# Kernel tuning notes

Hardware: AMD Instinct MI355X
Metric: run time of the kernel (lower is better)

The kernel has to match this reference:

```python
import math
import jax, jax.numpy as jnp
import numpy as np

C = 256          # channels
HID = 64         # max(int(C*0.25),16)
RH = 64          # max(C//4,32) router hidden
N, S, H, W = 8, 64, 16, 16
LOW_FREQ_RATIO = 0.2
ROUTER_TEMP = 1.0
LN_EPS = 1e-5

def gelu(v):
    return jax.nn.gelu(v, approximate=False)

def bn1d(v, s, b):  # folded eval-mode BatchNorm1d: (N,C,S)
    return v * s[None, :, None] + b[None, :, None]

def conv1x1(v, w, b=None):  # v:(N,Cin,S), w:(Cout,Cin)
    o = jnp.einsum('oc,ncs->nos', w, v)
    if b is not None:
        o = o + b[None, :, None]
    return o

def convk(v, w):  # v:(N,Cin,S), w:(Cout,Cin,K), 'same' padding
    k = w.shape[-1]
    return jax.lax.conv_general_dilated(v, w, (1,), [(k // 2, k // 2)],
                                        dimension_numbers=('NCH', 'OIH', 'NCH'))

def setup_inputs():
    key = jax.random.key(0)
    ks = iter(jax.random.split(key, 64))
    def nrm(shape, sc=0.02):
        return jax.random.normal(next(ks), shape, jnp.float32) * sc
    d = {}
    d['x'] = jax.random.normal(next(ks), (N, C, S, H, W), jnp.float32)
    d['ln_g'] = jnp.ones((C,), jnp.float32)
    d['ln_b'] = jnp.zeros((C,), jnp.float32)
    for k in (3, 5, 7):
        d['mb_w%d' % k] = nrm((C, 3 * C, k))
        d['mb_s%d' % k] = 1.0 + nrm((C,))
        d['mb_b%d' % k] = nrm((C,))
    d['mf_w'] = nrm((C, C)); d['mf_s'] = 1.0 + nrm((C,)); d['mf_b'] = nrm((C,))
    d['pg_w1'] = nrm((HID, 3)); d['pg_s1'] = 1.0 + nrm((HID,)); d['pg_b1'] = nrm((HID,))
    d['pg_w2'] = nrm((C, HID)); d['pg_b2'] = nrm((C,))
    d['pp_w'] = nrm((C, C)); d['pp_s'] = 1.0 + nrm((C,)); d['pp_b'] = nrm((C,))
    d['mg_w'] = nrm((C, 2 * C)); d['mg_b'] = nrm((C,))
    d['mo_w1'] = nrm((C, 3 * C)); d['mo_s1'] = 1.0 + nrm((C,)); d['mo_b1'] = nrm((C,))
    d['mo_w2'] = nrm((C, C))
    d['rt_w1'] = nrm((RH, C + 5)); d['rt_b1'] = nrm((RH,))
    d['rt_w2'] = nrm((3, RH)); d['rt_b2'] = nrm((3,))
    d['bp_w1'] = nrm((C, 4 * C)); d['bp_s1'] = 1.0 + nrm((C,)); d['bp_b1'] = nrm((C,))
    d['bp_w2'] = nrm((C, C))
    d['res_scale'] = jnp.full((1, C, 1), 0.05, jnp.float32)
    d['fg_w'] = nrm((C, C)); d['fg_b'] = nrm((C,))
    d['sg_w'] = nrm((C, C)); d['sg_s'] = 1.0 + nrm((C,)); d['sg_b'] = nrm((C,))
    return d

def _forward(x, ln_g, ln_b, mb_w3, mb_s3, mb_b3, mb_w5, mb_s5, mb_b5,
             mb_w7, mb_s7, mb_b7, mf_w, mf_s, mf_b,
             pg_w1, pg_s1, pg_b1, pg_w2, pg_b2, pp_w, pp_s, pp_b,
             mg_w, mg_b, mo_w1, mo_s1, mo_b1, mo_w2,
             rt_w1, rt_b1, rt_w2, rt_b2, bp_w1, bp_s1, bp_b1, bp_w2,
             res_scale, fg_w, fg_b, sg_w, sg_s, sg_b):
    n, c, s = x.shape[:3]
    x32 = x.astype(jnp.float32)
    desc = x32.mean(axis=(-1, -2))                     # (N,C,S)
    t = desc.transpose(0, 2, 1)                        # (N,S,C)
    mu = t.mean(-1, keepdims=True)
    var = t.var(-1, keepdims=True)
    dn = (((t - mu) / jnp.sqrt(var + LN_EPS)) * ln_g + ln_b).transpose(0, 2, 1)  # (N,C,S)

    def tdiff(v, order):
        dd = v[:, :, order:] - v[:, :, :-order]
        return jnp.pad(dd, ((0, 0), (0, 0), (order, 0)))
    diff1 = tdiff(dn, 1)
    diff2 = tdiff(dn, 2)

    # motion branch (multi-kernel conv1d + BN + GELU)
    mi = jnp.concatenate([dn, diff1, diff2], axis=1)   # (N,3C,S)
    motion = 0.0
    for w, bs, bb in ((mb_w3, mb_s3, mb_b3), (mb_w5, mb_s5, mb_b5), (mb_w7, mb_s7, mb_b7)):
        motion = motion + gelu(bn1d(convk(mi, w), bs, bb))
    motion = gelu(bn1d(conv1x1(motion / 3.0, mf_w), mf_s, mf_b))

    # FFT-based cycle / phase estimation
    tokens = dn.transpose(0, 2, 1)                     # (N,S,C)
    freq = jnp.fft.rfft(tokens, axis=1, norm='ortho')  # (N,F,C) complex
    fe = jnp.abs(freq).mean(-1)                        # (N,F)
    Fb = fe.shape[1]
    low = min(max(int(round(Fb * LOW_FREQ_RATIO)), 1), Fb - 1)
    he = fe[:, low:]
    peak_rel = jnp.argmax(he, axis=-1)                 # (N,)
    peak_idx = peak_rel + low
    peak_val = jnp.take_along_axis(he, peak_rel[:, None], axis=1)
    cycle_conf = peak_val / jnp.maximum(he.sum(axis=1, keepdims=True), 1e-6)  # (N,1)
    peak_norm = peak_idx.astype(jnp.float32)[:, None] / float(Fb - 1)
    mean_freq = freq.mean(-1)                          # (N,F) complex
    dom = jnp.take_along_axis(mean_freq, peak_idx[:, None], axis=1)[:, 0]
    dom_phase = jnp.arctan2(dom.imag, dom.real)
    tax = jnp.arange(s, dtype=jnp.float32)
    ang = (2.0 * math.pi / max(s, 1)) * peak_idx.astype(jnp.float32)
    arg = ang[:, None] * tax[None, :] + dom_phase[:, None]
    phase_cos = jnp.cos(arg)[:, None, :]               # (N,1,S)
    phase_sin = jnp.sin(arg)[:, None, :]

    cycle_token = jnp.broadcast_to(cycle_conf[:, :, None], (n, 1, s))
    pf = jnp.concatenate([phase_cos, phase_sin, cycle_token], axis=1)  # (N,3,S)
    pgate = jax.nn.sigmoid(conv1x1(gelu(bn1d(conv1x1(pf, pg_w1), pg_s1, pg_b1)), pg_w2, pg_b2))
    phase = gelu(bn1d(conv1x1(dn * pgate, pp_w), pp_s, pp_b))

    # bidirectional EMA memory via lax.scan
    gate = jax.nn.sigmoid(conv1x1(jnp.concatenate([dn, jnp.abs(diff1)], axis=1), mg_w, mg_b))
    g = gate.transpose(2, 0, 1)                        # (S,N,C)
    dd = dn.transpose(2, 0, 1)
    def step(st, gd):
        gt, dt = gd
        st = gt * st + (1.0 - gt) * dt
        return st, st
    _, fo = jax.lax.scan(step, dd[0], (g[1:], dd[1:]))
    fwd_mem = jnp.concatenate([dd[:1], fo], axis=0).transpose(1, 2, 0)
    _, bo = jax.lax.scan(step, dd[-1], (g[-2::-1], dd[-2::-1]))
    bwd_mem = jnp.concatenate([dd[-1:], bo], axis=0)[::-1].transpose(1, 2, 0)
    memory = conv1x1(gelu(bn1d(conv1x1(
        jnp.concatenate([dn, fwd_mem, bwd_mem], axis=1), mo_w1), mo_s1, mo_b1)), mo_w2)

    # router
    seq_std = dn.std(axis=2).mean(axis=1, keepdims=True)
    diff_energy = jnp.abs(diff1).mean(axis=(1, 2))[:, None]
    motion_energy = jnp.abs(motion).mean(axis=(1, 2))[:, None]
    memory_energy = jnp.abs(memory - dn).mean(axis=(1, 2))[:, None]
    stats = jnp.concatenate([seq_std, diff_energy, cycle_conf, peak_norm,
                             memory_energy + motion_energy], axis=-1)
    ri = jnp.concatenate([dn.mean(-1), stats], axis=-1)  # (N,C+5)
    hdn = gelu(ri @ rt_w1.T + rt_b1)
    logits = hdn @ rt_w2.T + rt_b2
    bw = jax.nn.softmax(logits / max(ROUTER_TEMP, 1e-6), axis=-1)  # (N,3)
    fused = (bw[:, 0, None, None] * motion + bw[:, 1, None, None] * phase
             + bw[:, 2, None, None] * memory)

    delta = conv1x1(gelu(bn1d(conv1x1(
        jnp.concatenate([dn, fused, motion - phase, memory - dn], axis=1),
        bp_w1), bp_s1, bp_b1)), bp_w2)
    delta = delta * jax.nn.sigmoid(conv1x1(dn, fg_w, fg_b))
    delta = res_scale * delta
    delta = delta[:, :, :, None, None]                 # (N,C,S,1,1)

    sp = x32.mean(axis=2)                              # (N,C,H,W)
    sg_lin = jnp.einsum('oc,nchw->nohw', sg_w, sp)
    sgate = jax.nn.sigmoid(sg_lin * sg_s[None, :, None, None] + sg_b[None, :, None, None])
    delta = delta * sgate[:, :, None, :, :]            # (N,C,S,H,W)
    return x + delta.astype(x.dtype)

def reference(x, ln_g, ln_b, mb_w3, mb_s3, mb_b3, mb_w5, mb_s5, mb_b5,
              mb_w7, mb_s7, mb_b7, mf_w, mf_s, mf_b,
              pg_w1, pg_s1, pg_b1, pg_w2, pg_b2, pp_w, pp_s, pp_b,
              mg_w, mg_b, mo_w1, mo_s1, mo_b1, mo_w2,
              rt_w1, rt_b1, rt_w2, rt_b2, bp_w1, bp_s1, bp_b1, bp_w2,
              res_scale, fg_w, fg_b, sg_w, sg_s, sg_b):
    return _forward(x, ln_g, ln_b, mb_w3, mb_s3, mb_b3, mb_w5, mb_s5, mb_b5,
                    mb_w7, mb_s7, mb_b7, mf_w, mf_s, mf_b,
                    pg_w1, pg_s1, pg_b1, pg_w2, pg_b2, pp_w, pp_s, pp_b,
                    mg_w, mg_b, mo_w1, mo_s1, mo_b1, mo_w2,
                    rt_w1, rt_b1, rt_w2, rt_b2, bp_w1, bp_s1, bp_b1, bp_w2,
                    res_scale, fg_w, fg_b, sg_w, sg_s, sg_b)
```

## Files before the change

### kernel.cpp

```cpp
#include <hip/hip_runtime.h>
#include <math.h>

namespace {

constexpr int N_ = 8, C_ = 256, S_ = 64, HW_ = 256;
constexpr int NS = N_ * S_;
constexpr int NHW = N_ * HW_;

constexpr size_t SZ_DESC = (size_t)NS * C_;
constexpr size_t O_DESC = 0;
constexpr size_t O_DN   = O_DESC + SZ_DESC;
constexpr size_t SZ_MIC = (size_t)N_ * 768 * 80;
constexpr size_t O_MIC  = O_DN + SZ_DESC;
constexpr size_t SZ_MPRE = (size_t)3 * 4 * 2048 * 64;
constexpr size_t O_MPRE = O_MIC + SZ_MIC;
constexpr size_t O_MSUM = O_MPRE + SZ_MPRE;
constexpr size_t O_MOT  = O_MSUM + SZ_DESC;
constexpr size_t SZ_GIB = (size_t)NS * 512;
constexpr size_t O_GIB  = O_MOT + SZ_DESC;
constexpr size_t O_GATE = O_GIB + SZ_GIB;
constexpr size_t SZ_MOI = (size_t)NS * 768;
constexpr size_t O_MOI  = O_GATE + SZ_DESC;
constexpr size_t O_HMO  = O_MOI + SZ_MOI;
constexpr size_t O_MEM  = O_HMO + SZ_DESC;
constexpr size_t O_PPIN = O_MEM + SZ_DESC;
constexpr size_t O_PHASE= O_PPIN + SZ_DESC;
constexpr size_t O_FGATE= O_PHASE + SZ_DESC;
constexpr size_t SZ_BPI = (size_t)NS * 1024;
constexpr size_t O_BPI  = O_FGATE + SZ_DESC;
constexpr size_t O_HBP  = O_BPI + SZ_BPI;
constexpr size_t O_DELTA= O_HBP + SZ_DESC;
constexpr size_t SZ_SPT = (size_t)NHW * C_;
constexpr size_t O_SPT  = O_DELTA + SZ_DESC;
constexpr size_t O_SGATE= O_SPT + SZ_SPT;
constexpr size_t O_FE   = O_SGATE + SZ_SPT;
constexpr size_t O_MFRE = O_FE + 512;
constexpr size_t O_MFIM = O_MFRE + 512;
constexpr size_t O_PK   = O_MFIM + 512;
constexpr size_t O_BW   = O_PK + 32;
constexpr size_t SZ_WT3 = (size_t)768*3*256;
constexpr size_t O_WT3  = O_BW + 32;
constexpr size_t SZ_WT5 = (size_t)768*5*256;
constexpr size_t O_WT5  = O_WT3 + SZ_WT3;
constexpr size_t SZ_WT7 = (size_t)768*7*256;
constexpr size_t O_WT7  = O_WT5 + SZ_WT5;
constexpr size_t O_ATMF = O_WT7 + SZ_WT7;
constexpr size_t O_ATMG = O_ATMF + 256*256;
constexpr size_t O_ATMO1= O_ATMG + 512*256;
constexpr size_t O_ATMO2= O_ATMO1 + 768*256;
constexpr size_t O_ATPP = O_ATMO2 + 256*256;
constexpr size_t O_ATBP1= O_ATPP + 256*256;
constexpr size_t O_ATBP2= O_ATBP1 + 1024*256;
constexpr size_t O_ATFG = O_ATBP2 + 256*256;
constexpr size_t O_ATSG = O_ATFG + 256*256;

__device__ __forceinline__ float gelu_f(float v) {
  return 0.5f * v * (1.0f + erff(v * 0.70710678118654752f));
}
__device__ __forceinline__ float sigmoid_f(float v) {
  return 1.0f / (1.0f + expf(-v));
}

__device__ __forceinline__ float block_sum256(float v, float* scratch) {
  #pragma unroll
  for (int off = 32; off; off >>= 1) v += __shfl_down(v, off, 64);
  int w = threadIdx.x >> 6;
  __syncthreads();
  if ((threadIdx.x & 63) == 0) scratch[w] = v;
  __syncthreads();
  return scratch[0] + scratch[1] + scratch[2] + scratch[3];
}

__global__ __launch_bounds__(256) void transpose_kernel(
    const float* __restrict__ w3, const float* __restrict__ w5, const float* __restrict__ w7,
    const float* __restrict__ wmf, const float* __restrict__ wmg,
    const float* __restrict__ wmo1, const float* __restrict__ wmo2,
    const float* __restrict__ wpp, const float* __restrict__ wbp1,
    const float* __restrict__ wbp2, const float* __restrict__ wfg,
    const float* __restrict__ wsg, float* __restrict__ ws) {
  __shared__ float tile[32][33];
  int xt = blockIdx.x, yt = blockIdx.y;
  const float* src; float* dst; int K;
  if      (xt < 72)  { src = w3;   dst = ws + O_WT3;   K = 2304; }
  else if (xt < 192) { src = w5;   dst = ws + O_WT5;   K = 3840; xt -= 72; }
  else if (xt < 360) { src = w7;   dst = ws + O_WT7;   K = 5376; xt -= 192; }
  else if (xt < 368) { src = wmf;  dst = ws + O_ATMF;  K = 256;  xt -= 360; }
  else if (xt < 384) { src = wmg;  dst = ws + O_ATMG;  K = 512;  xt -= 368; }
  else if (xt < 408) { src = wmo1; dst = ws + O_ATMO1; K = 768;  xt -= 384; }
  else if (xt < 416) { src = wmo2; dst = ws + O_ATMO2; K = 256;  xt -= 408; }
  else if (xt < 424) { src = wpp;  dst = ws + O_ATPP;  K = 256;  xt -= 416; }
  else if (xt < 456) { src = wbp1; dst = ws + O_ATBP1; K = 1024; xt -= 424; }
  else if (xt < 464) { src = wbp2; dst = ws + O_ATBP2; K = 256;  xt -= 456; }
  else if (xt < 472) { src = wfg;  dst = ws + O_ATFG;  K = 256;  xt -= 464; }
  else               { src = wsg;  dst = ws + O_ATSG;  K = 256;  xt -= 472; }
  int tx = threadIdx.x & 31, ty = threadIdx.x >> 5;
  int c = xt * 32 + tx;
  #pragma unroll
  for (int i = 0; i < 4; ++i) {
    int r = yt * 32 + ty + i * 8;
    tile[ty + i * 8][tx] = src[(size_t)r * K + c];
  }
  __syncthreads();
  #pragma unroll
  for (int i = 0; i < 4; ++i) {
    int cc = xt * 32 + ty + i * 8;
    dst[(size_t)cc * 256 + yt * 32 + tx] = tile[tx][ty + i * 8];
  }
}

__global__ __launch_bounds__(256) void reduce_x_kernel(
    const float* __restrict__ x, float* __restrict__ desc_t, float* __restrict__ sp_t) {
  int nc = blockIdx.x; int n = nc >> 8; int c = nc & 255;
  int t = threadIdx.x; int w = t >> 6; int l = t & 63;
  const float4* x4 = (const float4*)x + (size_t)nc * 4096;
  float4 sa = {0.f, 0.f, 0.f, 0.f};
  for (int i = 0; i < 16; ++i) {
    int s = w * 16 + i;
    float4 v = x4[(size_t)s * 64 + l];
    sa.x += v.x; sa.y += v.y; sa.z += v.z; sa.w += v.w;
    float ds = v.x + v.y + v.z + v.w;
    #pragma unroll
    for (int off = 32; off; off >>= 1) ds += __shfl_down(ds, off, 64);
    if (l == 0) desc_t[((size_t)n * 64 + s) * 256 + c] = ds * (1.f / 256.f);
  }
  __shared__ float4 lsp[4][64];
  lsp[w][l] = sa;
  __syncthreads();
  if (t < 64) {
    float4 a = lsp[0][t], b = lsp[1][t], c2 = lsp[2][t], d = lsp[3][t];
    float4 tot;
    tot.x = a.x + b.x + c2.x + d.x; tot.y = a.y + b.y + c2.y + d.y;
    tot.z = a.z + b.z + c2.z + d.z; tot.w = a.w + b.w + c2.w + d.w;
    size_t base = ((size_t)n * 256 + t * 4) * 256 + c;
    sp_t[base]       = tot.x * (1.f / 64.f);
    sp_t[base + 256] = tot.y * (1.f / 64.f);
    sp_t[base + 512] = tot.z * (1.f / 64.f);
    sp_t[base + 768] = tot.w * (1.f / 64.f);
  }
}

__global__ __launch_bounds__(256) void ln_kernel(
    const float* __restrict__ desc_t, const float* __restrict__ g,
    const float* __restrict__ b, float* __restrict__ dn_t) {
  __shared__ float sc[4];
  int col = blockIdx.x; int t = threadIdx.x;
  float v = desc_t[(size_t)col * 256 + t];
  float s1 = block_sum256(v, sc);
  float s2 = block_sum256(v * v, sc);
  float mu = s1 * (1.f / 256.f);
  float var = s2 * (1.f / 256.f) - mu * mu;
  float r = rsqrtf(var + 1e-5f);
  dn_t[(size_t)col * 256 + t] = (v - mu) * r * g[t] + b[t];
}

__global__ __launch_bounds__(256) void prep_mi_kernel(
    const float* __restrict__ dn_t, float* __restrict__ mi_c,
    float* __restrict__ gib, float* __restrict__ moi, float* __restrict__ bpi) {
  int col = blockIdx.x; int c = threadIdx.x;
  int n = col >> 6, s = col & 63;
  float d = dn_t[(size_t)col * 256 + c];
  float d1 = (s >= 1) ? d - dn_t[(size_t)(col - 1) * 256 + c] : 0.f;
  float d2 = (s >= 2) ? d - dn_t[(size_t)(col - 2) * 256 + c] : 0.f;
  size_t r0 = ((size_t)n * 768 + c) * 80;
  size_t r1 = ((size_t)n * 768 + 256 + c) * 80;
  size_t r2 = ((size_t)n * 768 + 512 + c) * 80;
  mi_c[r0 + 8 + s] = d; mi_c[r1 + 8 + s] = d1; mi_c[r2 + 8 + s] = d2;
  if (s < 8)  { mi_c[r0 + s] = 0.f; mi_c[r1 + s] = 0.f; mi_c[r2 + s] = 0.f; }
  if (s >= 56){ int p = 72 + (s - 56); mi_c[r0 + p] = 0.f; mi_c[r1 + p] = 0.f; mi_c[r2 + p] = 0.f; }
  gib[(size_t)col * 512 + c] = d;
  gib[(size_t)col * 512 + 256 + c] = fabsf(d1);
  moi[(size_t)col * 768 + c] = d;
  bpi[(size_t)col * 1024 + c] = d;
}

__global__ __launch_bounds__(256) void fft_kernel(
    const float* __restrict__ dn_t, float* __restrict__ fe,
    float* __restrict__ mfre, float* __restrict__ mfim) {
  int b = blockIdx.x; int n = b / 33; int f = b % 33;
  int t = threadIdx.x;
  __shared__ float cs[64], sn[64];
  __shared__ float sc[4];
  if (t < 64) {
    int ft = (f * t) & 63;
    float ang = -6.283185307179586f * (float)ft * (1.f / 64.f);
    cs[t] = cosf(ang); sn[t] = sinf(ang);
  }
  __syncthreads();
  float re = 0.f, im = 0.f;
  const float* base = dn_t + (size_t)n * 16384 + t;
  for (int s = 0; s < 64; ++s) {
    float v = base[(size_t)s * 256];
    re += v * cs[s]; im += v * sn[s];
  }
  re *= 0.125f; im *= 0.125f;
  float mag = sqrtf(re * re + im * im);
  float sm = block_sum256(mag, sc);
  float sr = block_sum256(re, sc);
  float si = block_sum256(im, sc);
  if (t == 0) {
    fe[b]   = sm * (1.f / 256.f);
    mfre[b] = sr * (1.f / 256.f);
    mfim[b] = si * (1.f / 256.f);
  }
}

__global__ __launch_bounds__(64) void peak_kernel(
    const float* __restrict__ fe, const float* __restrict__ mfre,
    const float* __restrict__ mfim, float* __restrict__ pk) {
  int n = blockIdx.x; int t = threadIdx.x;
  float v = (t < 26) ? fe[n * 33 + 7 + t] : -1e30f;
  int idx = t;
  float hs = (t < 26) ? v : 0.f;
  #pragma unroll
  for (int off = 32; off; off >>= 1) {
    float ov = __shfl_down(v, off, 64);
    int   oi = __shfl_down(idx, off, 64);
    float oh = __shfl_down(hs, off, 64);
    hs += oh;
    if (ov > v || (ov == v && oi < idx)) { v = ov; idx = oi; }
  }
  if (t == 0) {
    int pi = idx + 7;
    float conf = v / fmaxf(hs, 1e-6f);
    float pnorm = (float)pi * (1.f / 32.f);
    float re = mfre[n * 33 + pi], im = mfim[n * 33 + pi];
    float dph = atan2f(im, re);
    float ang = (6.283185307179586f / 64.f) * (float)pi;
    pk[n * 4 + 0] = conf; pk[n * 4 + 1] = pnorm; pk[n * 4 + 2] = dph; pk[n * 4 + 3] = ang;
  }
}

__global__ __launch_bounds__(256) void conv_fused_kernel(
    const float* __restrict__ mi_c, const float* __restrict__ wt3,
    const float* __restrict__ wt5, const float* __restrict__ wt7,
    float* __restrict__ mpre) {
  int n = blockIdx.x, part = blockIdx.y, ot = blockIdx.z;
  int t = threadIdx.x;
  __shared__ float lmi[192 * 80];
  {
    const float4* src = (const float4*)(mi_c + ((size_t)n * 768 + part * 192) * 80);
    float4* dst = (float4*)lmi;
    #pragma unroll
    for (int i = 0; i < 15; ++i) dst[t + i * 256] = src[t + i * 256];
  }
  __syncthreads();
  int o = ot * 32 + (t & 31);
  int s0 = (t >> 5) * 8;
  float a3[8], a5[8], a7[8];
  #pragma unroll
  for (int j = 0; j < 8; ++j) { a3[j] = 0.f; a5[j] = 0.f; a7[j] = 0.f; }
  const float* w3p = wt3 + (size_t)(part * 192 * 3) * 256 + o;
  const float* w5p = wt5 + (size_t)(part * 192 * 5) * 256 + o;
  const float* w7p = wt7 + (size_t)(part * 192 * 7) * 256 + o;
  const float* lrow = lmi + 8 + s0 - 3;
  for (int ic = 0; ic < 192; ++ic) {
    float win[14];
    #pragma unroll
    for (int j = 0; j < 14; ++j) win[j] = lrow[ic * 80 + j];
    #pragma unroll
    for (int dk = 0; dk < 7; ++dk) {
      float w = w7p[(size_t)(ic * 7 + dk) * 256];
      #pragma unroll
      for (int j = 0; j < 8; ++j) a7[j] = fmaf(w, win[dk + j], a7[j]);
    }
    #pragma unroll
    for (int dk = 0; dk < 5; ++dk) {
      float w = w5p[(size_t)(ic * 5 + dk) * 256];
      #pragma unroll
      for (int j = 0; j < 8; ++j) a5[j] = fmaf(w, win[1 + dk + j], a5[j]);
    }
    #pragma unroll
    for (int dk = 0; dk < 3; ++dk) {
      float w = w3p[(size_t)(ic * 3 + dk) * 256];
      #pragma unroll
      for (int j = 0; j < 8; ++j) a3[j] = fmaf(w, win[2 + dk + j], a3[j]);
    }
  }
  size_t base = ((size_t)part * 2048 + n * 256 + o) * 64 + s0;
  #pragma unroll
  for (int j = 0; j < 8; ++j) {
    mpre[base + j]           = a3[j];
    mpre[base + 524288 + j]  = a5[j];
    mpre[base + 1048576 + j] = a7[j];
  }
}

__global__ __launch_bounds__(256) void combine_kernel(
    const float* __restrict__ mpre,
    const float* __restrict__ s3, const float* __restrict__ b3,
    const float* __restrict__ s5, const float* __restrict__ b5,
    const float* __restrict__ s7, const float* __restrict__ b7,
    float* __restrict__ msum) {
  int id = blockIdx.x * 256 + threadIdx.x;
  int s = id & 63; int o = (id >> 6) & 255; int n = id >> 14;
  size_t base = ((size_t)n * 256 + o) * 64 + s;
  float v0 = mpre[base] + mpre[base + 131072] + mpre[base + 262144] + mpre[base + 393216];
  size_t b5o = base + 524288;
  float v1 = mpre[b5o] + mpre[b5o + 131072] + mpre[b5o + 262144] + mpre[b5o + 393216];
  size_t b7o = base + 1048576;
  float v2 = mpre[b7o] + mpre[b7o + 131072] + mpre[b7o + 262144] + mpre[b7o + 393216];
  float tot = gelu_f(v0 * s3[o] + b3[o]) + gelu_f(v1 * s5[o] + b5[o]) + gelu_f(v2 * s7[o] + b7[o]);
  msum[((size_t)n * 64 + s) * 256 + o] = tot * (1.f / 3.f);
}

template <int K, int EPI>
__global__ __launch_bounds__(256) void gemm_kernel(
    const float* __restrict__ At, const float* __restrict__ B, float* __restrict__ out,
    const float* __restrict__ sc, const float* __restrict__ bi,
    const float* __restrict__ fg, const float* __restrict__ rs) {
  int t = threadIdx.x;
  int o = blockIdx.x * 64 + (t & 63);
  int c0 = blockIdx.y * 8 + (t >> 6) * 2;
  const float* b0p = B + (size_t)c0 * K;
  const float* b1p = b0p + K;
  float4 a0 = {0.f,0.f,0.f,0.f}, a1 = {0.f,0.f,0.f,0.f};
  for (int kk = 0; kk < K; kk += 4) {
    float4 b0 = *(const float4*)(b0p + kk);
    float4 b1 = *(const float4*)(b1p + kk);
    float w0 = At[(size_t)(kk + 0) * 256 + o];
    float w1 = At[(size_t)(kk + 1) * 256 + o];
    float w2 = At[(size_t)(kk + 2) * 256 + o];
    float w3 = At[(size_t)(kk + 3) * 256 + o];
    a0.x += w0 * b0.x; a0.y += w1 * b0.y; a0.z += w2 * b0.z; a0.w += w3 * b0.w;
    a1.x += w0 * b1.x; a1.y += w1 * b1.y; a1.z += w2 * b1.z; a1.w += w3 * b1.w;
  }
  float v0 = (a0.x + a0.y) + (a0.z + a0.w);
  float v1 = (a1.x + a1.y) + (a1.z + a1.w);
  if constexpr (EPI == 0) { v0 = gelu_f(v0 * sc[o] + bi[o]); v1 = gelu_f(v1 * sc[o] + bi[o]); }
  else if constexpr (EPI == 1) { v0 = sigmoid_f(v0 + bi[o]); v1 = sigmoid_f(v1 + bi[o]); }
  else if constexpr (EPI == 3) {
    v0 *= fg[(size_t)c0 * 256 + o] * rs[o];
    v1 *= fg[(size_t)(c0 + 1) * 256 + o] * rs[o];
  }
  else if constexpr (EPI == 4) { v0 = sigmoid_f(v0 * sc[o] + bi[o]); v1 = sigmoid_f(v1 * sc[o] + bi[o]); }
  out[(size_t)c0 * 256 + o] = v0;
  out[(size_t)(c0 + 1) * 256 + o] = v1;
}

__global__ __launch_bounds__(256) void scan_kernel(
    const float* __restrict__ dn_t, const float* __restrict__ gate_t, float* __restrict__ moi) {
  int n = blockIdx.x, half = blockIdx.y;
  int t = threadIdx.x;
  __shared__ float ld[64 * 128];
  __shared__ float lg[64 * 128];
  const float* dsrc = dn_t + (size_t)n * 16384 + half * 128;
  const float* gsrc = gate_t + (size_t)n * 16384 + half * 128;
  for (int i = t; i < 8192; i += 256) {
    int s = i >> 7, j = i & 127;
    ld[i] = dsrc[(size_t)s * 256 + j];
    lg[i] = gsrc[(size_t)s * 256 + j];
  }
  __syncthreads();
  int cl = t & 127;
  int c = half * 128 + cl;
  size_t ob = (size_t)n * 64 * 768 + c;
  if (t < 128) {
    float st = ld[cl];
    moi[ob + 256] = st;
    for (int s = 1; s < 64; ++s) {
      float g = lg[s * 128 + cl], d = ld[s * 128 + cl];
      st = g * st + (1.f - g) * d;
      moi[ob + (size_t)s * 768 + 256] = st;
    }
  } else {
    float st = ld[63 * 128 + cl];
    moi[ob + (size_t)63 * 768 + 512] = st;
    for (int s = 62; s >= 0; --s) {
      float g = lg[s * 128 + cl], d = ld[s * 128 + cl];
      st = g * st + (1.f - g) * d;
      moi[ob + (size_t)s * 768 + 512] = st;
    }
  }
}

__global__ __launch_bounds__(256) void pgate_kernel(
    const float* __restrict__ dn_t, const float* __restrict__ pk,
    const float* __restrict__ pg_w1, const float* __restrict__ pg_s1, const float* __restrict__ pg_b1,
    const float* __restrict__ pg_w2, const float* __restrict__ pg_b2, float* __restrict__ ppin) {
  int col = blockIdx.x; int n = col >> 6; int s = col & 63;
  int t = threadIdx.x;
  __shared__ float h[64];
  float conf = pk[n * 4 + 0], dph = pk[n * 4 + 2], ang = pk[n * 4 + 3];
  float arg = ang * (float)s + dph;
  float pc = cosf(arg), ps = sinf(arg);
  if (t < 64) {
    float v = pg_w1[t * 3 + 0] * pc + pg_w1[t * 3 + 1] * ps + pg_w1[t * 3 + 2] * conf;
    v = v * pg_s1[t] + pg_b1[t];
    h[t] = gelu_f(v);
  }
  __syncthreads();
  float acc = pg_b2[t];
  const float* wrow = pg_w2 + t * 64;
  #pragma unroll 8
  for (int j = 0; j < 64; ++j) acc += wrow[j] * h[j];
  float pg = sigmoid_f(acc);
  ppin[(size_t)col * 256 + t] = dn_t[(size_t)col * 256 + t] * pg;
}

__global__ __launch_bounds__(256) void router_kernel(
    const float* __restrict__ dn_t, const float* __restrict__ motion_t,
    const float* __restrict__ memory_t, const float* __restrict__ pk,
    const float* __restrict__ rt_w1, const float* __restrict__ rt_b1,
    const float* __restrict__ rt_w2, const float* __restrict__ rt_b2,
    float* __restrict__ bw) {
  int n = blockIdx.x; int c = threadIdx.x;
  __shared__ float ri[261];
  __shared__ float h2[64];
  __shared__ float lg[3];
  __shared__ float sc[4];
  float sum = 0.f, sq = 0.f, ad1 = 0.f, amot = 0.f, amem = 0.f, prev = 0.f;
  for (int s = 0; s < 64; ++s) {
    size_t i = ((size_t)n * 64 + s) * 256 + c;
    float d = dn_t[i];
    sum += d; sq += d * d;
    if (s > 0) ad1 += fabsf(d - prev);
    prev = d;
    amot += fabsf(motion_t[i]);
    amem += fabsf(memory_t[i] - d);
  }
// ... 43 lines not shown
  int col = blockIdx.x; int c = threadIdx.x; int n = col >> 6;
  size_t i = (size_t)col * 256 + c;
  float m = motion_t[i], p = phase_t[i], me = memory_t[i], d = dn_t[i];
  float b0 = bw[n * 3 + 0], b1 = bw[n * 3 + 1], b2 = bw[n * 3 + 2];
  size_t base = (size_t)col * 1024;
  bpi[base + 256 + c] = b0 * m + b1 * p + b2 * me;
  bpi[base + 512 + c] = m - p;
  bpi[base + 768 + c] = me - d;
}

__global__ __launch_bounds__(256) void final_kernel(
    const float* __restrict__ x, const float* __restrict__ delta_t,
    const float* __restrict__ sgate_t, float* __restrict__ out) {
  int nc = blockIdx.x; int n = nc >> 8; int c = nc & 255;
  int t = threadIdx.x;
  __shared__ float dlt[64];
  __shared__ float4 sgs4[64];
  if (t < 64) dlt[t] = delta_t[((size_t)n * 64 + t) * 256 + c];
  ((float*)sgs4)[t] = sgate_t[((size_t)n * 256 + t) * 256 + c];
  __syncthreads();
  const float4* x4 = (const float4*)x + (size_t)nc * 4096;
  float4* o4 = (float4*)out + (size_t)nc * 4096;
  int w = t >> 6, l = t & 63;
  float4 sg = sgs4[l];
  for (int i = 0; i < 16; ++i) {
    int s = w * 16 + i;
    float d = dlt[s];
    float4 v = x4[(size_t)s * 64 + l];
    v.x += d * sg.x; v.y += d * sg.y; v.z += d * sg.z; v.w += d * sg.w;
    o4[(size_t)s * 64 + l] = v;
  }
}

}

extern "C" void kernel_launch(void* const* d_in, const int* in_sizes, int n_in,
                              void* d_out, int out_size, void* d_ws, size_t ws_size,
                              hipStream_t stream) {
  const float* x      = (const float*)d_in[0];
  const float* ln_g   = (const float*)d_in[1];
  const float* ln_b   = (const float*)d_in[2];
  const float* mb_w3  = (const float*)d_in[3];
  const float* mb_s3  = (const float*)d_in[4];
  const float* mb_b3  = (const float*)d_in[5];
  const float* mb_w5  = (const float*)d_in[6];
  const float* mb_s5  = (const float*)d_in[7];
  const float* mb_b5  = (const float*)d_in[8];
  const float* mb_w7  = (const float*)d_in[9];
  const float* mb_s7  = (const float*)d_in[10];
  const float* mb_b7  = (const float*)d_in[11];
  const float* mf_w   = (const float*)d_in[12];
  const float* mf_s   = (const float*)d_in[13];
  const float* mf_b   = (const float*)d_in[14];
  const float* pg_w1  = (const float*)d_in[15];
  const float* pg_s1  = (const float*)d_in[16];
  const float* pg_b1  = (const float*)d_in[17];
  const float* pg_w2  = (const float*)d_in[18];
  const float* pg_b2  = (const float*)d_in[19];
  const float* pp_w   = (const float*)d_in[20];
  const float* pp_s   = (const float*)d_in[21];
  const float* pp_b   = (const float*)d_in[22];
  const float* mg_w   = (const float*)d_in[23];
  const float* mg_b   = (const float*)d_in[24];
  const float* mo_w1  = (const float*)d_in[25];
  const float* mo_s1  = (const float*)d_in[26];
  const float* mo_b1  = (const float*)d_in[27];
  const float* mo_w2  = (const float*)d_in[28];
  const float* rt_w1  = (const float*)d_in[29];
  const float* rt_b1  = (const float*)d_in[30];
  const float* rt_w2  = (const float*)d_in[31];
  const float* rt_b2  = (const float*)d_in[32];
  const float* bp_w1  = (const float*)d_in[33];
  const float* bp_s1  = (const float*)d_in[34];
  const float* bp_b1  = (const float*)d_in[35];
  const float* bp_w2  = (const float*)d_in[36];
  const float* res_sc = (const float*)d_in[37];
  const float* fg_w   = (const float*)d_in[38];
  const float* fg_b   = (const float*)d_in[39];
  const float* sg_w   = (const float*)d_in[40];
  const float* sg_s   = (const float*)d_in[41];
  const float* sg_b   = (const float*)d_in[42];
  float* ws = (float*)d_ws;
  float* out = (float*)d_out;

  transpose_kernel<<<dim3(480, 8), 256, 0, stream>>>(mb_w3, mb_w5, mb_w7, mf_w, mg_w,
      mo_w1, mo_w2, pp_w, bp_w1, bp_w2, fg_w, sg_w, ws);
  reduce_x_kernel<<<2048, 256, 0, stream>>>(x, ws + O_DESC, ws + O_SPT);
  ln_kernel<<<512, 256, 0, stream>>>(ws + O_DESC, ln_g, ln_b, ws + O_DN);
  prep_mi_kernel<<<512, 256, 0, stream>>>(ws + O_DN, ws + O_MIC, ws + O_GIB, ws + O_MOI, ws + O_BPI);
  fft_kernel<<<264, 256, 0, stream>>>(ws + O_DN, ws + O_FE, ws + O_MFRE, ws + O_MFIM);
  peak_kernel<<<8, 64, 0, stream>>>(ws + O_FE, ws + O_MFRE, ws + O_MFIM, ws + O_PK);
  conv_fused_kernel<<<dim3(8, 4, 8), 256, 0, stream>>>(ws + O_MIC, ws + O_WT3, ws + O_WT5, ws + O_WT7, ws + O_MPRE);
  combine_kernel<<<512, 256, 0, stream>>>(ws + O_MPRE, mb_s3, mb_b3, mb_s5, mb_b5, mb_s7, mb_b7, ws + O_MSUM);
  gemm_kernel<256, 0><<<dim3(4, 64), 256, 0, stream>>>(ws + O_ATMF, ws + O_MSUM, ws + O_MOT, mf_s, mf_b, nullptr, nullptr);
  gemm_kernel<512, 1><<<dim3(4, 64), 256, 0, stream>>>(ws + O_ATMG, ws + O_GIB, ws + O_GATE, nullptr, mg_b, nullptr, nullptr);
  scan_kernel<<<dim3(8, 2), 256, 0, stream>>>(ws + O_DN, ws + O_GATE, ws + O_MOI);
  gemm_kernel<768, 0><<<dim3(4, 64), 256, 0, stream>>>(ws + O_ATMO1, ws + O_MOI, ws + O_HMO, mo_s1, mo_b1, nullptr, nullptr);
  gemm_kernel<256, 2><<<dim3(4, 64), 256, 0, stream>>>(ws + O_ATMO2, ws + O_HMO, ws + O_MEM, nullptr, nullptr, nullptr, nullptr);
  pgate_kernel<<<512, 256, 0, stream>>>(ws + O_DN, ws + O_PK, pg_w1, pg_s1, pg_b1, pg_w2, pg_b2, ws + O_PPIN);
  gemm_kernel<256, 0><<<dim3(4, 64), 256, 0, stream>>>(ws + O_ATPP, ws + O_PPIN, ws + O_PHASE, pp_s, pp_b, nullptr, nullptr);
  gemm_kernel<256, 1><<<dim3(4, 64), 256, 0, stream>>>(ws + O_ATFG, ws + O_DN, ws + O_FGATE, nullptr, fg_b, nullptr, nullptr);
  router_kernel<<<8, 256, 0, stream>>>(ws + O_DN, ws + O_MOT, ws + O_MEM, ws + O_PK,
      rt_w1, rt_b1, rt_w2, rt_b2, ws + O_BW);
  bp_prep_kernel<<<512, 256, 0, stream>>>(ws + O_MOT, ws + O_PHASE, ws + O_MEM, ws + O_DN, ws + O_BW, ws + O_BPI);
  gemm_kernel<1024, 0><<<dim3(4, 64), 256, 0, stream>>>(ws + O_ATBP1, ws + O_BPI, ws + O_HBP, bp_s1, bp_b1, nullptr, nullptr);
  gemm_kernel<256, 3><<<dim3(4, 64), 256, 0, stream>>>(ws + O_ATBP2, ws + O_HBP, ws + O_DELTA, nullptr, nullptr, ws + O_FGATE, res_sc);
  gemm_kernel<256, 4><<<dim3(4, 256), 256, 0, stream>>>(ws + O_ATSG, ws + O_SPT, ws + O_SGATE, sg_s, sg_b, nullptr, nullptr);
  final_kernel<<<2048, 256, 0, stream>>>(x, ws + O_DELTA, ws + O_SGATE, out);
}
```

Baseline: 699.4 us.

## Replace FP32 multi-scale conv with bf16 MFMA im2col GEMM and split-K

The three 1D convolutions (kernel sizes 3, 5 and 7) become a single im2col GEMM. Weights are zero-padded to a common 7-tap layout and repacked into bf16 MFMA fragments, and the conv runs on 16x16x32 bf16 matrix instructions with 4-way split-K. A transposing combine kernel then sums the partial results and applies BN and GELU. Separately, the generic FP32 GEMM now computes one column per thread with twice as many blocks, to raise parallelism. The bf16 inputs add rounding error, and the weight repacking runs on every call.

```diff
diff --git a/kernel.cpp b/kernel.cpp
--- a/kernel.cpp
+++ b/kernel.cpp
@@ -7,52 +7,44 @@
 constexpr int NS = N_ * S_;
 constexpr int NHW = N_ * HW_;
 
-constexpr size_t SZ_DESC = (size_t)NS * C_;
-constexpr size_t O_DESC = 0;
-constexpr size_t O_DN   = O_DESC + SZ_DESC;
-constexpr size_t SZ_MIC = (size_t)N_ * 768 * 80;
-constexpr size_t O_MIC  = O_DN + SZ_DESC;
-constexpr size_t SZ_MPRE = (size_t)3 * 4 * 2048 * 64;
-constexpr size_t O_MPRE = O_MIC + SZ_MIC;
-constexpr size_t O_MSUM = O_MPRE + SZ_MPRE;
-constexpr size_t O_MOT  = O_MSUM + SZ_DESC;
-constexpr size_t SZ_GIB = (size_t)NS * 512;
-constexpr size_t O_GIB  = O_MOT + SZ_DESC;
-constexpr size_t O_GATE = O_GIB + SZ_GIB;
-constexpr size_t SZ_MOI = (size_t)NS * 768;
-constexpr size_t O_MOI  = O_GATE + SZ_DESC;
-constexpr size_t O_HMO  = O_MOI + SZ_MOI;
-constexpr size_t O_MEM  = O_HMO + SZ_DESC;
-constexpr size_t O_PPIN = O_MEM + SZ_DESC;
-constexpr size_t O_PHASE= O_PPIN + SZ_DESC;
-constexpr size_t O_FGATE= O_PHASE + SZ_DESC;
-constexpr size_t SZ_BPI = (size_t)NS * 1024;
-constexpr size_t O_BPI  = O_FGATE + SZ_DESC;
-constexpr size_t O_HBP  = O_BPI + SZ_BPI;
-constexpr size_t O_DELTA= O_HBP + SZ_DESC;
-constexpr size_t SZ_SPT = (size_t)NHW * C_;
-constexpr size_t O_SPT  = O_DELTA + SZ_DESC;
-constexpr size_t O_SGATE= O_SPT + SZ_SPT;
-constexpr size_t O_FE   = O_SGATE + SZ_SPT;
-constexpr size_t O_MFRE = O_FE + 512;
-constexpr size_t O_MFIM = O_MFRE + 512;
-constexpr size_t O_PK   = O_MFIM + 512;
-constexpr size_t O_BW   = O_PK + 32;
-constexpr size_t SZ_WT3 = (size_t)768*3*256;
-constexpr size_t O_WT3  = O_BW + 32;
-constexpr size_t SZ_WT5 = (size_t)768*5*256;
-constexpr size_t O_WT5  = O_WT3 + SZ_WT3;
-constexpr size_t SZ_WT7 = (size_t)768*7*256;
-constexpr size_t O_WT7  = O_WT5 + SZ_WT5;
-constexpr size_t O_ATMF = O_WT7 + SZ_WT7;
-constexpr size_t O_ATMG = O_ATMF + 256*256;
-constexpr size_t O_ATMO1= O_ATMG + 512*256;
-constexpr size_t O_ATMO2= O_ATMO1 + 768*256;
-constexpr size_t O_ATPP = O_ATMO2 + 256*256;
-constexpr size_t O_ATBP1= O_ATPP + 256*256;
-constexpr size_t O_ATBP2= O_ATBP1 + 1024*256;
-constexpr size_t O_ATFG = O_ATBP2 + 256*256;
-constexpr size_t O_ATSG = O_ATFG + 256*256;
+constexpr size_t O_DESC  = 0;
+constexpr size_t O_DN    = 131072;
+constexpr size_t O_MSUM  = 262144;
+constexpr size_t O_MOT   = 393216;
+constexpr size_t O_GATE  = 524288;
+constexpr size_t O_HMO   = 655360;
+constexpr size_t O_MEM   = 786432;
+constexpr size_t O_PPIN  = 917504;
+constexpr size_t O_PHASE = 1048576;
+constexpr size_t O_FGATE = 1179648;
+constexpr size_t O_HBP   = 1310720;
+constexpr size_t O_DELTA = 1441792;
+constexpr size_t O_GIB   = 1572864;
+constexpr size_t O_MOI   = 1835008;
+constexpr size_t O_BPI   = 2228224;
+constexpr size_t O_SPT   = 2752512;
+constexpr size_t O_SGATE = 3276800;
+constexpr size_t O_FE    = 3801088;
+constexpr size_t O_MFRE  = 3801600;
+constexpr size_t O_MFIM  = 3802112;
+constexpr size_t O_PK    = 3802624;
+constexpr size_t O_BW    = 3802656;
+constexpr size_t O_ATMF  = 3802688;
+constexpr size_t O_ATMG  = 3868224;
+constexpr size_t O_ATMO1 = 3999296;
+constexpr size_t O_ATMO2 = 4195904;
+constexpr size_t O_ATPP  = 4261440;
+constexpr size_t O_ATBP1 = 4326976;
+constexpr size_t O_ATBP2 = 4589120;
+constexpr size_t O_ATFG  = 4654656;
+constexpr size_t O_ATSG  = 4720192;
+constexpr size_t O_WFRAG = 4785728;
+constexpr size_t O_IM2   = 6850112;
+constexpr size_t O_CONVC = 8226368;
+
+typedef __attribute__((ext_vector_type(4))) float f32x4;
+typedef __attribute__((ext_vector_type(8))) short s16x8;
+typedef __attribute__((ext_vector_type(8))) unsigned short u16x8;
 
 __device__ __forceinline__ float gelu_f(float v) {
   return 0.5f * v * (1.0f + erff(v * 0.70710678118654752f));
@@ -60,6 +52,11 @@
 __device__ __forceinline__ float sigmoid_f(float v) {
   return 1.0f / (1.0f + expf(-v));
 }
+__device__ __forceinline__ unsigned short f2bf(float f) {
+  unsigned int u = __float_as_uint(f);
+  u += 0x7fffu + ((u >> 16) & 1u);
+  return (unsigned short)(u >> 16);
+}
 
 __device__ __forceinline__ float block_sum256(float v, float* scratch) {
   #pragma unroll
@@ -72,7 +69,6 @@
 }
 
 __global__ __launch_bounds__(256) void transpose_kernel(
-    const float* __restrict__ w3, const float* __restrict__ w5, const float* __restrict__ w7,
     const float* __restrict__ wmf, const float* __restrict__ wmg,
     const float* __restrict__ wmo1, const float* __restrict__ wmo2,
     const float* __restrict__ wpp, const float* __restrict__ wbp1,
@@ -81,18 +77,15 @@
   __shared__ float tile[32][33];
   int xt = blockIdx.x, yt = blockIdx.y;
   const float* src; float* dst; int K;
-  if      (xt < 72)  { src = w3;   dst = ws + O_WT3;   K = 2304; }
-  else if (xt < 192) { src = w5;   dst = ws + O_WT5;   K = 3840; xt -= 72; }
-  else if (xt < 360) { src = w7;   dst = ws + O_WT7;   K = 5376; xt -= 192; }
-  else if (xt < 368) { src = wmf;  dst = ws + O_ATMF;  K = 256;  xt -= 360; }
-  else if (xt < 384) { src = wmg;  dst = ws + O_ATMG;  K = 512;  xt -= 368; }
-  else if (xt < 408) { src = wmo1; dst = ws + O_ATMO1; K = 768;  xt -= 384; }
-  else if (xt < 416) { src = wmo2; dst = ws + O_ATMO2; K = 256;  xt -= 408; }
-  else if (xt < 424) { src = wpp;  dst = ws + O_ATPP;  K = 256;  xt -= 416; }
-  else if (xt < 456) { src = wbp1; dst = ws + O_ATBP1; K = 1024; xt -= 424; }
-  else if (xt < 464) { src = wbp2; dst = ws + O_ATBP2; K = 256;  xt -= 456; }
-  else if (xt < 472) { src = wfg;  dst = ws + O_ATFG;  K = 256;  xt -= 464; }
-  else               { src = wsg;  dst = ws + O_ATSG;  K = 256;  xt -= 472; }
+  if      (xt < 8)   { src = wmf;  dst = ws + O_ATMF;  K = 256;  }
+  else if (xt < 24)  { src = wmg;  dst = ws + O_ATMG;  K = 512;  xt -= 8;  }
+  else if (xt < 48)  { src = wmo1; dst = ws + O_ATMO1; K = 768;  xt -= 24; }
+  else if (xt < 56)  { src = wmo2; dst = ws + O_ATMO2; K = 256;  xt -= 48; }
+  else if (xt < 64)  { src = wpp;  dst = ws + O_ATPP;  K = 256;  xt -= 56; }
+  else if (xt < 96)  { src = wbp1; dst = ws + O_ATBP1; K = 1024; xt -= 64; }
+  else if (xt < 104) { src = wbp2; dst = ws + O_ATBP2; K = 256;  xt -= 96; }
+  else if (xt < 112) { src = wfg;  dst = ws + O_ATFG;  K = 256;  xt -= 104;}
+  else               { src = wsg;  dst = ws + O_ATSG;  K = 256;  xt -= 112;}
   int tx = threadIdx.x & 31, ty = threadIdx.x >> 5;
   int c = xt * 32 + tx;
   #pragma unroll
@@ -105,6 +98,135 @@
   for (int i = 0; i < 4; ++i) {
     int cc = xt * 32 + ty + i * 8;
     dst[(size_t)cc * 256 + yt * 32 + tx] = tile[tx][ty + i * 8];
+  }
+}
+
+__global__ __launch_bounds__(256) void wfrag_kernel(
+    const float* __restrict__ w3, const float* __restrict__ w5, const float* __restrict__ w7,
+    unsigned short* __restrict__ wf) {
+  int g = blockIdx.x * 256 + threadIdx.x;
+  int lane = g & 63;
+  int m16 = (g >> 6) % 48;
+  int kchunk = (g >> 6) / 48;
+  int o = m16 * 16 + (lane & 15);
+  int conv = o >> 8, oc = o & 255;
+  int q = lane >> 4;
+  u16x8 out;
+  #pragma unroll
+  for (int j = 0; j < 8; ++j) {
+    int k = kchunk * 32 + q * 8 + j;
+    int ic = k / 7;
+    int tau = k - ic * 7 - 3;
+    float v = 0.f;
+    if (conv == 0) {
+      if (tau >= -1 && tau <= 1) v = w3[((size_t)oc * 768 + ic) * 3 + (tau + 1)];
+    } else if (conv == 1) {
+      if (tau >= -2 && tau <= 2) v = w5[((size_t)oc * 768 + ic) * 5 + (tau + 2)];
+    } else {
+      v = w7[((size_t)oc * 768 + ic) * 7 + (tau + 3)];
+    }
+    out[j] = f2bf(v);
+  }
+  *((u16x8*)wf + g) = out;
+}
+
+__global__ __launch_bounds__(256) void im2col_kernel(
+    const float* __restrict__ dn_t, unsigned short* __restrict__ imf) {
+  int g = blockIdx.x * 256 + threadIdx.x;
+  int lane = g & 63;
+  int c16 = (g >> 6) % 32;
+  int kchunk = (g >> 6) / 32;
+  int col = c16 * 16 + (lane & 15);
+  int n = col >> 6, s = col & 63;
+  int q = lane >> 4;
+  const float* base = dn_t + (size_t)n * 16384;
+  u16x8 out;
+  #pragma unroll
+  for (int j = 0; j < 8; ++j) {
+    int k = kchunk * 32 + q * 8 + j;
+    int ic = k / 7;
+    int tau = k - ic * 7 - 3;
+    int stream = ic >> 8, c = ic & 255;
+    int sp = s + tau;
+    float v = 0.f;
+    if (sp >= 0 && sp < 64) {
+      float d = base[(size_t)sp * 256 + c];
+      if (stream == 0) v = d;
+      else if (stream == 1) v = (sp >= 1) ? d - base[(size_t)(sp - 1) * 256 + c] : 0.f;
+      else v = (sp >= 2) ? d - base[(size_t)(sp - 2) * 256 + c] : 0.f;
+    }
+    out[j] = f2bf(v);
+  }
+  *((u16x8*)imf + g) = out;
+}
+
+__global__ __launch_bounds__(256) void conv_mfma_kernel(
+    const unsigned short* __restrict__ wf, const unsigned short* __restrict__ imf,
+    float* __restrict__ partial) {
+  int mt = blockIdx.x, nt = blockIdx.y, kp = blockIdx.z;
+  int lane = threadIdx.x & 63;
+  int w = threadIdx.x >> 6;
+  int m16 = mt * 4 + w;
+  const s16x8* wfp = (const s16x8*)wf;
+  const s16x8* imp = (const s16x8*)imf;
+  f32x4 acc0 = {0.f,0.f,0.f,0.f}, acc1 = {0.f,0.f,0.f,0.f};
+  f32x4 acc2 = {0.f,0.f,0.f,0.f}, acc3 = {0.f,0.f,0.f,0.f};
+  #pragma unroll 2
+  for (int cc = 0; cc < 42; ++cc) {
+    int kc = kp * 42 + cc;
+    s16x8 a = wfp[(size_t)(kc * 48 + m16) * 64 + lane];
+    s16x8 b0 = imp[(size_t)(kc * 32 + nt * 4 + 0) * 64 + lane];
+    s16x8 b1 = imp[(size_t)(kc * 32 + nt * 4 + 1) * 64 + lane];
+    s16x8 b2 = imp[(size_t)(kc * 32 + nt * 4 + 2) * 64 + lane];
+    s16x8 b3 = imp[(size_t)(kc * 32 + nt * 4 + 3) * 64 + lane];
+    acc0 = __builtin_amdgcn_mfma_f32_16x16x32_bf16(a, b0, acc0, 0, 0, 0);
+    acc1 = __builtin_amdgcn_mfma_f32_16x16x32_bf16(a, b1, acc1, 0, 0, 0);
+    acc2 = __builtin_amdgcn_mfma_f32_16x16x32_bf16(a, b2, acc2, 0, 0, 0);
+    acc3 = __builtin_amdgcn_mfma_f32_16x16x32_bf16(a, b3, acc3, 0, 0, 0);
+  }
+  int q = lane >> 4, ln = lane & 15;
+  int o0 = m16 * 16 + q * 4;
+  float* pb = partial + (size_t)kp * 393216;
+  #pragma unroll
+  for (int r = 0; r < 4; ++r) {
+    size_t row = (size_t)(o0 + r) * 512;
+    pb[row + (nt * 4 + 0) * 16 + ln] = acc0[r];
+    pb[row + (nt * 4 + 1) * 16 + ln] = acc1[r];
+    pb[row + (nt * 4 + 2) * 16 + ln] = acc2[r];
+    pb[row + (nt * 4 + 3) * 16 + ln] = acc3[r];
+  }
+}
+
+__global__ __launch_bounds__(256) void combine_kernel(
+    const float* __restrict__ P,
+    const float* __restrict__ s3, const float* __restrict__ b3,
+    const float* __restrict__ s5, const float* __restrict__ b5,
+    const float* __restrict__ s7, const float* __restrict__ b7,
+    float* __restrict__ msum) {
+  __shared__ float tile[32][33];
+  int col0 = blockIdx.x * 32, o0 = blockIdx.y * 32;
+  int t = threadIdx.x;
+  int cl = t & 31, orow = t >> 5;
+  #pragma unroll
+  for (int p = 0; p < 4; ++p) {
+    int ol = p * 8 + orow;
+    int o = o0 + ol, col = col0 + cl;
+    float v3 = 0.f, v5 = 0.f, v7 = 0.f;
+    #pragma unroll
+    for (int kpp = 0; kpp < 4; ++kpp) {
+      size_t base = (size_t)kpp * 393216 + col;
+      v3 += P[base + (size_t)o * 512];
+      v5 += P[base + (size_t)(o + 256) * 512];
+      v7 += P[base + (size_t)(o + 512) * 512];
+    }
+    float tot = gelu_f(v3 * s3[o] + b3[o]) + gelu_f(v5 * s5[o] + b5[o]) + gelu_f(v7 * s7[o] + b7[o]);
+    tile[ol][cl] = tot * (1.f / 3.f);
+  }
+  __syncthreads();
+  #pragma unroll
+  for (int p = 0; p < 4; ++p) {
+    int coll = p * 8 + orow;
+    msum[(size_t)(col0 + coll) * 256 + o0 + cl] = tile[cl][coll];
   }
 }
 
@@ -154,19 +276,12 @@
 }
 
 __global__ __launch_bounds__(256) void prep_mi_kernel(
-    const float* __restrict__ dn_t, float* __restrict__ mi_c,
+    const float* __restrict__ dn_t,
     float* __restrict__ gib, float* __restrict__ moi, float* __restrict__ bpi) {
   int col = blockIdx.x; int c = threadIdx.x;
-  int n = col >> 6, s = col & 63;
+  int s = col & 63;
   float d = dn_t[(size_t)col * 256 + c];
   float d1 = (s >= 1) ? d - dn_t[(size_t)(col - 1) * 256 + c] : 0.f;
-  float d2 = (s >= 2) ? d - dn_t[(size_t)(col - 2) * 256 + c] : 0.f;
-  size_t r0 = ((size_t)n * 768 + c) * 80;
-  size_t r1 = ((size_t)n * 768 + 256 + c) * 80;
-  size_t r2 = ((size_t)n * 768 + 512 + c) * 80;
-  mi_c[r0 + 8 + s] = d; mi_c[r1 + 8 + s] = d1; mi_c[r2 + 8 + s] = d2;
-  if (s < 8)  { mi_c[r0 + s] = 0.f; mi_c[r1 + s] = 0.f; mi_c[r2 + s] = 0.f; }
-  if (s >= 56){ int p = 72 + (s - 56); mi_c[r0 + p] = 0.f; mi_c[r1 + p] = 0.f; mi_c[r2 + p] = 0.f; }
   gib[(size_t)col * 512 + c] = d;
   gib[(size_t)col * 512 + 256 + c] = fabsf(d1);
   moi[(size_t)col * 768 + c] = d;
@@ -230,79 +345,6 @@
   }
 }
 
-__global__ __launch_bounds__(256) void conv_fused_kernel(
-    const float* __restrict__ mi_c, const float* __restrict__ wt3,
-    const float* __restrict__ wt5, const float* __restrict__ wt7,
-    float* __restrict__ mpre) {
-  int n = blockIdx.x, part = blockIdx.y, ot = blockIdx.z;
-  int t = threadIdx.x;
-  __shared__ float lmi[192 * 80];
-  {
-    const float4* src = (const float4*)(mi_c + ((size_t)n * 768 + part * 192) * 80);
-    float4* dst = (float4*)lmi;
-    #pragma unroll
-    for (int i = 0; i < 15; ++i) dst[t + i * 256] = src[t + i * 256];
-  }
-  __syncthreads();
-  int o = ot * 32 + (t & 31);
-  int s0 = (t >> 5) * 8;
-  float a3[8], a5[8], a7[8];
-  #pragma unroll
-  for (int j = 0; j < 8; ++j) { a3[j] = 0.f; a5[j] = 0.f; a7[j] = 0.f; }
-  const float* w3p = wt3 + (size_t)(part * 192 * 3) * 256 + o;
-  const float* w5p = wt5 + (size_t)(part * 192 * 5) * 256 + o;
-  const float* w7p = wt7 + (size_t)(part * 192 * 7) * 256 + o;
-  const float* lrow = lmi + 8 + s0 - 3;
-  for (int ic = 0; ic < 192; ++ic) {
-    float win[14];
-    #pragma unroll
-    for (int j = 0; j < 14; ++j) win[j] = lrow[ic * 80 + j];
-    #pragma unroll
-    for (int dk = 0; dk < 7; ++dk) {
-      float w = w7p[(size_t)(ic * 7 + dk) * 256];
-      #pragma unroll
-      for (int j = 0; j < 8; ++j) a7[j] = fmaf(w, win[dk + j], a7[j]);
-    }
-    #pragma unroll
-    for (int dk = 0; dk < 5; ++dk) {
-      float w = w5p[(size_t)(ic * 5 + dk) * 256];
-      #pragma unroll
-      for (int j = 0; j < 8; ++j) a5[j] = fmaf(w, win[1 + dk + j], a5[j]);
-    }
-    #pragma unroll
-    for (int dk = 0; dk < 3; ++dk) {
-      float w = w3p[(size_t)(ic * 3 + dk) * 256];
-      #pragma unroll
-      for (int j = 0; j < 8; ++j) a3[j] = fmaf(w, win[2 + dk + j], a3[j]);
-    }
-  }
-  size_t base = ((size_t)part * 2048 + n * 256 + o) * 64 + s0;
-  #pragma unroll
-  for (int j = 0; j < 8; ++j) {
-    mpre[base + j]           = a3[j];
-    mpre[base + 524288 + j]  = a5[j];
-    mpre[base + 1048576 + j] = a7[j];
-  }
-}
-
-__global__ __launch_bounds__(256) void combine_kernel(
-    const float* __restrict__ mpre,
-    const float* __restrict__ s3, const float* __restrict__ b3,
-    const float* __restrict__ s5, const float* __restrict__ b5,
-    const float* __restrict__ s7, const float* __restrict__ b7,
-    float* __restrict__ msum) {
-  int id = blockIdx.x * 256 + threadIdx.x;
-  int s = id & 63; int o = (id >> 6) & 255; int n = id >> 14;
-  size_t base = ((size_t)n * 256 + o) * 64 + s;
-  float v0 = mpre[base] + mpre[base + 131072] + mpre[base + 262144] + mpre[base + 393216];
-  size_t b5o = base + 524288;
-  float v1 = mpre[b5o] + mpre[b5o + 131072] + mpre[b5o + 262144] + mpre[b5o + 393216];
-  size_t b7o = base + 1048576;
-  float v2 = mpre[b7o] + mpre[b7o + 131072] + mpre[b7o + 262144] + mpre[b7o + 393216];
-  float tot = gelu_f(v0 * s3[o] + b3[o]) + gelu_f(v1 * s5[o] + b5[o]) + gelu_f(v2 * s7[o] + b7[o]);
-  msum[((size_t)n * 64 + s) * 256 + o] = tot * (1.f / 3.f);
-}
-
 template <int K, int EPI>
 __global__ __launch_bounds__(256) void gemm_kernel(
     const float* __restrict__ At, const float* __restrict__ B, float* __restrict__ out,
@@ -310,31 +352,22 @@
     const float* __restrict__ fg, const float* __restrict__ rs) {
   int t = threadIdx.x;
   int o = blockIdx.x * 64 + (t & 63);
-  int c0 = blockIdx.y * 8 + (t >> 6) * 2;
-  const float* b0p = B + (size_t)c0 * K;
-  const float* b1p = b0p + K;
-  float4 a0 = {0.f,0.f,0.f,0.f}, a1 = {0.f,0.f,0.f,0.f};
+  int col = blockIdx.y * 4 + (t >> 6);
+  const float* bp = B + (size_t)col * K;
+  float4 a0 = {0.f,0.f,0.f,0.f};
   for (int kk = 0; kk < K; kk += 4) {
-    float4 b0 = *(const float4*)(b0p + kk);
-    float4 b1 = *(const float4*)(b1p + kk);
-    float w0 = At[(size_t)(kk + 0) * 256 + o];
-    float w1 = At[(size_t)(kk + 1) * 256 + o];
-    float w2 = At[(size_t)(kk + 2) * 256 + o];
-    float w3 = At[(size_t)(kk + 3) * 256 + o];
-    a0.x += w0 * b0.x; a0.y += w1 * b0.y; a0.z += w2 * b0.z; a0.w += w3 * b0.w;
-    a1.x += w0 * b1.x; a1.y += w1 * b1.y; a1.z += w2 * b1.z; a1.w += w3 * b1.w;
+    float4 b0 = *(const float4*)(bp + kk);
+    a0.x += At[(size_t)(kk + 0) * 256 + o] * b0.x;
+    a0.y += At[(size_t)(kk + 1) * 256 + o] * b0.y;
+    a0.z += At[(size_t)(kk + 2) * 256 + o] * b0.z;
+    a0.w += At[(size_t)(kk + 3) * 256 + o] * b0.w;
   }
   float v0 = (a0.x + a0.y) + (a0.z + a0.w);
-  float v1 = (a1.x + a1.y) + (a1.z + a1.w);
-  if constexpr (EPI == 0) { v0 = gelu_f(v0 * sc[o] + bi[o]); v1 = gelu_f(v1 * sc[o] + bi[o]); }
-  else if constexpr (EPI == 1) { v0 = sigmoid_f(v0 + bi[o]); v1 = sigmoid_f(v1 + bi[o]); }
-  else if constexpr (EPI == 3) {
-    v0 *= fg[(size_t)c0 * 256 + o] * rs[o];
-    v1 *= fg[(size_t)(c0 + 1) * 256 + o] * rs[o];
-  }
-  else if constexpr (EPI == 4) { v0 = sigmoid_f(v0 * sc[o] + bi[o]); v1 = sigmoid_f(v1 * sc[o] + bi[o]); }
-  out[(size_t)c0 * 256 + o] = v0;
-  out[(size_t)(c0 + 1) * 256 + o] = v1;
+  if constexpr (EPI == 0) { v0 = gelu_f(v0 * sc[o] + bi[o]); }
+  else if constexpr (EPI == 1) { v0 = sigmoid_f(v0 + bi[o]); }
+  else if constexpr (EPI == 3) { v0 *= fg[(size_t)col * 256 + o] * rs[o]; }
+  else if constexpr (EPI == 4) { v0 = sigmoid_f(v0 * sc[o] + bi[o]); }
+  out[(size_t)col * 256 + o] = v0;
 }
 
 __global__ __launch_bounds__(256) void scan_kernel(
@@ -544,29 +577,33 @@
   const float* sg_b   = (const float*)d_in[42];
   float* ws = (float*)d_ws;
   float* out = (float*)d_out;
-
-  transpose_kernel<<<dim3(480, 8), 256, 0, stream>>>(mb_w3, mb_w5, mb_w7, mf_w, mg_w,
-      mo_w1, mo_w2, pp_w, bp_w1, bp_w2, fg_w, sg_w, ws);
+  unsigned short* wfrag = (unsigned short*)(ws + O_WFRAG);
+  unsigned short* im2   = (unsigned short*)(ws + O_IM2);
+
+  transpose_kernel<<<dim3(120, 8), 256, 0, stream>>>(mf_w, mg_w, mo_w1, mo_w2,
+      pp_w, bp_w1, bp_w2, fg_w, sg_w, ws);
+  wfrag_kernel<<<2016, 256, 0, stream>>>(mb_w3, mb_w5, mb_w7, wfrag);
   reduce_x_kernel<<<2048, 256, 0, stream>>>(x, ws + O_DESC, ws + O_SPT);
   ln_kernel<<<512, 256, 0, stream>>>(ws + O_DESC, ln_g, ln_b, ws + O_DN);
-  prep_mi_kernel<<<512, 256, 0, stream>>>(ws + O_DN, ws + O_MIC, ws + O_GIB, ws + O_MOI, ws + O_BPI);
+  im2col_kernel<<<1344, 256, 0, stream>>>(ws + O_DN, im2);
+  prep_mi_kernel<<<512, 256, 0, stream>>>(ws + O_DN, ws + O_GIB, ws + O_MOI, ws + O_BPI);
   fft_kernel<<<264, 256, 0, stream>>>(ws + O_DN, ws + O_FE, ws + O_MFRE, ws + O_MFIM);
   peak_kernel<<<8, 64, 0, stream>>>(ws + O_FE, ws + O_MFRE, ws + O_MFIM, ws + O_PK);
-  conv_fused_kernel<<<dim3(8, 4, 8), 256, 0, stream>>>(ws + O_MIC, ws + O_WT3, ws + O_WT5, ws + O_WT7, ws + O_MPRE);
-  combine_kernel<<<512, 256, 0, stream>>>(ws + O_MPRE, mb_s3, mb_b3, mb_s5, mb_b5, mb_s7, mb_b7, ws + O_MSUM);
-  gemm_kernel<256, 0><<<dim3(4, 64), 256, 0, stream>>>(ws + O_ATMF, ws + O_MSUM, ws + O_MOT, mf_s, mf_b, nullptr, nullptr);
-  gemm_kernel<512, 1><<<dim3(4, 64), 256, 0, stream>>>(ws + O_ATMG, ws + O_GIB, ws + O_GATE, nullptr, mg_b, nullptr, nullptr);
+  conv_mfma_kernel<<<dim3(12, 8, 4), 256, 0, stream>>>(wfrag, im2, ws + O_CONVC);
+  combine_kernel<<<dim3(16, 8), 256, 0, stream>>>(ws + O_CONVC, mb_s3, mb_b3, mb_s5, mb_b5, mb_s7, mb_b7, ws + O_MSUM);
+  gemm_kernel<256, 0><<<dim3(4, 128), 256, 0, stream>>>(ws + O_ATMF, ws + O_MSUM, ws + O_MOT, mf_s, mf_b, nullptr, nullptr);
+  gemm_kernel<512, 1><<<dim3(4, 128), 256, 0, stream>>>(ws + O_ATMG, ws + O_GIB, ws + O_GATE, nullptr, mg_b, nullptr, nullptr);
   scan_kernel<<<dim3(8, 2), 256, 0, stream>>>(ws + O_DN, ws + O_GATE, ws + O_MOI);
-  gemm_kernel<768, 0><<<dim3(4, 64), 256, 0, stream>>>(ws + O_ATMO1, ws + O_MOI, ws + O_HMO, mo_s1, mo_b1, nullptr, nullptr);
-  gemm_kernel<256, 2><<<dim3(4, 64), 256, 0, stream>>>(ws + O_ATMO2, ws + O_HMO, ws + O_MEM, nullptr, nullptr, nullptr, nullptr);
+  gemm_kernel<768, 0><<<dim3(4, 128), 256, 0, stream>>>(ws + O_ATMO1, ws + O_MOI, ws + O_HMO, mo_s1, mo_b1, nullptr, nullptr);
+  gemm_kernel<256, 2><<<dim3(4, 128), 256, 0, stream>>>(ws + O_ATMO2, ws + O_HMO, ws + O_MEM, nullptr, nullptr, nullptr, nullptr);
   pgate_kernel<<<512, 256, 0, stream>>>(ws + O_DN, ws + O_PK, pg_w1, pg_s1, pg_b1, pg_w2, pg_b2, ws + O_PPIN);
-  gemm_kernel<256, 0><<<dim3(4, 64), 256, 0, stream>>>(ws + O_ATPP, ws + O_PPIN, ws + O_PHASE, pp_s, pp_b, nullptr, nullptr);
-  gemm_kernel<256, 1><<<dim3(4, 64), 256, 0, stream>>>(ws + O_ATFG, ws + O_DN, ws + O_FGATE, nullptr, fg_b, nullptr, nullptr);
+  gemm_kernel<256, 0><<<dim3(4, 128), 256, 0, stream>>>(ws + O_ATPP, ws + O_PPIN, ws + O_PHASE, pp_s, pp_b, nullptr, nullptr);
+  gemm_kernel<256, 1><<<dim3(4, 128), 256, 0, stream>>>(ws + O_ATFG, ws + O_DN, ws + O_FGATE, nullptr, fg_b, nullptr, nullptr);
   router_kernel<<<8, 256, 0, stream>>>(ws + O_DN, ws + O_MOT, ws + O_MEM, ws + O_PK,
       rt_w1, rt_b1, rt_w2, rt_b2, ws + O_BW);
   bp_prep_kernel<<<512, 256, 0, stream>>>(ws + O_MOT, ws + O_PHASE, ws + O_MEM, ws + O_DN, ws + O_BW, ws + O_BPI);
-  gemm_kernel<1024, 0><<<dim3(4, 64), 256, 0, stream>>>(ws + O_ATBP1, ws + O_BPI, ws + O_HBP, bp_s1, bp_b1, nullptr, nullptr);
-  gemm_kernel<256, 3><<<dim3(4, 64), 256, 0, stream>>>(ws + O_ATBP2, ws + O_HBP, ws + O_DELTA, nullptr, nullptr, ws + O_FGATE, res_sc);
-  gemm_kernel<256, 4><<<dim3(4, 256), 256, 0, stream>>>(ws + O_ATSG, ws + O_SPT, ws + O_SGATE, sg_s, sg_b, nullptr, nullptr);
+  gemm_kernel<1024, 0><<<dim3(4, 128), 256, 0, stream>>>(ws + O_ATBP1, ws + O_BPI, ws + O_HBP, bp_s1, bp_b1, nullptr, nullptr);
+  gemm_kernel<256, 3><<<dim3(4, 128), 256, 0, stream>>>(ws + O_ATBP2, ws + O_HBP, ws + O_DELTA, nullptr, nullptr, ws + O_FGATE, res_sc);
+  gemm_kernel<256, 4><<<dim3(4, 512), 256, 0, stream>>>(ws + O_ATSG, ws + O_SPT, ws + O_SGATE, sg_s, sg_b, nullptr, nullptr);
   final_kernel<<<2048, 256, 0, stream>>>(x, ws + O_DELTA, ws + O_SGATE, out);
 }
```

New measurement: 604.8 us. 1.16x faster.
